# Kernel optimization log

Hardware: AMD Instinct MI355X
Metric: run time of the kernel (lower is better)

Reference implementation:

```python
import jax, jax.numpy as jnp
import numpy as np

H = 128          # hidden_size
GX = GY = 512    # grid_size
SW = 2           # spatial_width
NX = GX + 3 * SW # memory extent x (as in SpatialExternalMemory ctor)
NY = GY + 3 * SW
B = 512          # batch (num trajectories)
T = 64           # seq len (recurrent steps)


def setup_inputs() -> dict:
    key = jax.random.key(0)
    ks = jax.random.split(key, 9)
    stdv = 1.0 / np.sqrt(H)
    feat = jax.random.normal(ks[0], (B, T, 2), jnp.float32)
    # integer grid coords stored as floats in cols 2:4 (cast to long in forward)
    coords = jax.random.randint(ks[1], (B, T, 2), 0, GX).astype(jnp.float32)
    feature_tensor = jnp.concatenate([feat, coords], axis=-1)  # [B, T, 4]
    seq_lengths = jax.random.randint(ks[2], (B,), 1, T + 1)
    uni = lambda k, shp: jax.random.uniform(k, shp, jnp.float32, -stdv, stdv)
    return {
        "feature_tensor": feature_tensor,
        "W_ih": uni(ks[3], (4 * H, 2)),
        "b_ih": uni(ks[4], (4 * H,)),
        "W_hh": uni(ks[5], (4 * H, H)),
        "b_hh": uni(ks[6], (4 * H,)),
        "W_out": uni(ks[7], (H, 2 * H)),   # Attention.linear_out: [H, 2H]
        "b_out": uni(ks[8], (H,)),
        "seq_lengths": seq_lengths,
    }


def reference(feature_tensor, W_ih, b_ih, W_hh, b_hh, W_out, b_out, seq_lengths):
    step_idx = jnp.maximum(seq_lengths.astype(jnp.int32), 1) - 1  # [B]
    offsets = jnp.arange(-SW, SW + 1)                              # [K], K=2*SW+1
    K = 2 * SW + 1
    memory0 = jnp.zeros((NX, NY, H), jnp.float32)
    hidden0 = jnp.zeros((B, H), jnp.float32)
    last0 = jnp.zeros((B, H), jnp.float32)

    def step(carry, inp):
        hidden, memory, last = carry
        xt, t = inp                                 # xt: [B,4]
        feat = xt[:, :2]
        grid = xt[:, 2:4].astype(jnp.int32) + SW    # [B,2]
        gi = feat @ W_ih.T + b_ih                   # [B,4H]
        gh = hidden @ W_hh.T + b_hh                 # [B,4H]
        i_r, i_i, i_n, i_s = jnp.split(gi, 4, axis=1)
        h_r, h_i, h_n, h_s = jnp.split(gh, 4, axis=1)
        resetgate = jax.nn.sigmoid(i_r + h_r)
        updategate = jax.nn.sigmoid(i_i + h_i)
        spatialgate = jax.nn.sigmoid(i_s + h_s)
        newgate = jnp.tanh(i_n + resetgate * h_n)
        # --- find_nearby_grids: 5x5 neighborhood gather ---
        gx = jnp.clip(grid[:, 0], 0, NX - 1)
        gy = jnp.clip(grid[:, 1], 0, NY - 1)
        xi = jnp.clip(gx[:, None] + offsets[None, :], 0, NX - 1)   # [B,K]
        yi = jnp.clip(gy[:, None] + offsets[None, :], 0, NY - 1)   # [B,K]
        xg = jnp.broadcast_to(xi[:, :, None], (B, K, K)).reshape(B, K * K)
        yg = jnp.broadcast_to(yi[:, None, :], (B, K, K)).reshape(B, K * K)
        context = memory[xg, yg]                    # [B, K*K, H]
        # --- Attention(newgate.detach(), context) ---
        q = jax.lax.stop_gradient(newgate)
        scores = jnp.einsum('bh,bkh->bk', q, context)
        scores = jnp.where(scores == 0.0, -jnp.inf, scores)
        attn = jax.nn.softmax(scores, axis=1)
        attn = jnp.where(jnp.isnan(attn), 0.0, attn)
        mix = jnp.einsum('bk,bkh->bh', attn, context)
        atten_cs = jnp.tanh(jnp.concatenate([mix, q], axis=-1) @ W_out.T + b_out)
        curr = newgate + spatialgate * atten_cs
        out = curr + updategate * (hidden - curr)
        # --- in-cell memory write (detached, training-mode path) ---
        sd = jax.lax.stop_gradient(spatialgate)
        od = jax.lax.stop_gradient(out)
        upd = sd * memory[gx, gy] + (1.0 - sd) * od
        memory = memory.at[gx, gy].set(upd)
        last = jnp.where((step_idx == t)[:, None], out, last)
        return (out, memory, last), None

    xs = (jnp.swapaxes(feature_tensor, 0, 1), jnp.arange(T))
    (_, _, last), _ = jax.lax.scan(step, (hidden0, memory0, last0), xs)
    return last
```

## Files before the change

kernel.cpp:

```cpp
#include <hip/hip_runtime.h>
#include <hip/hip_fp16.h>
#include <math.h>

#define Hc   128
#define Bc   512
#define Tc   64
#define NXc  518
#define NCELL (518*518)
#define NEV  (Bc*Tc)
#define SWc  2


__global__ void k_build(const float* __restrict__ feat, int* __restrict__ head,
                        int* __restrict__ nxt, int* __restrict__ cellxy) {
    int gid = blockIdx.x * 256 + threadIdx.x;
    if (gid >= NEV) return;
    int b = gid >> 6, t = gid & 63;
    int base = (b * Tc + t) * 4;
    int gx = (int)feat[base + 2] + SWc;
    int gy = (int)feat[base + 3] + SWc;
    gx = min(max(gx, 0), NXc - 1);
    gy = min(max(gy, 0), NXc - 1);
    int cell = gx * NXc + gy;
    int e = t * Bc + b;
    cellxy[e] = (gx << 16) | gy;
    int old = atomicExch(&head[cell], e);
    nxt[e] = old;
}

__global__ void k_resolve(const int* __restrict__ head, const int* __restrict__ nxt,
                          const int* __restrict__ cellxy, int* __restrict__ dep) {
    int gid = blockIdx.x * 256 + threadIdx.x;
    if (gid >= NEV * 25) return;
    int r = gid / 25, k = gid - r * 25;
    int t = r & 63, b = r >> 6;
    int e0 = t * Bc + b;
    int xy = cellxy[e0];
    int gx = xy >> 16, gy = xy & 0xffff;
    int cx = gx + (k / 5) - SWc, cy = gy + (k % 5) - SWc;
    cx = min(max(cx, 0), NXc - 1);
    cy = min(max(cy, 0), NXc - 1);
    int cell = cx * NXc + cy;
    int best = -1;
    for (int e = head[cell]; e >= 0; e = nxt[e])
        if ((e >> 9) < t && e > best) best = e;
    dep[r * 25 + k] = best;
}


#define LOG2E 1.4426950408889634f
__device__ __forceinline__ float fexp(float x)  { return __builtin_amdgcn_exp2f(x * LOG2E); }
__device__ __forceinline__ float fsig(float x)  { return __builtin_amdgcn_rcpf(1.f + fexp(-x)); }
__device__ __forceinline__ float ftanh(float x) { return 1.f - 2.f * __builtin_amdgcn_rcpf(1.f + fexp(2.f * x)); }

__device__ __forceinline__ void barlds() {
    asm volatile("" ::: "memory");
    __builtin_amdgcn_s_waitcnt(0xC07F);
    __builtin_amdgcn_s_barrier();
    asm volatile("" ::: "memory");
}


constexpr int LDS_FLOATS = 16512 + 256 + 1024 + 256 + 256 + 256 + 64 + 2048 + 512 + 16 + 128 + 256 + 128;
constexpr int LDS_BYTES  = LDS_FLOATS * 4;

__global__ void
__attribute__((amdgpu_flat_work_group_size(1024, 1024)))
__attribute__((amdgpu_waves_per_eu(4, 4)))
step_main(const float* __restrict__ feat, const float* __restrict__ Wih,
          const float* __restrict__ bih,  const float* __restrict__ Whh,
          const float* __restrict__ bhh,  const float* __restrict__ Wout,
          const float* __restrict__ bout, const int*   __restrict__ seq,
          const int*   __restrict__ dep,  float* __restrict__ vbuf,
          unsigned*    __restrict__ flags, float* __restrict__ dout) {
    extern __shared__ float lds[];
    __half2* WoutH = (__half2*)lds;
    float* hid   = lds + 16512;
    float* g     = hid   + 256;
    float* gin   = g     + 1024;
    float* ctr   = gin   + 256;
    float* qvL   = ctr   + 256;
    float* scor  = qvL   + 256;
    float* pmix  = scor  + 64;
    float* catL  = pmix  + 2048;
    float* fxy   = catL  + 512;
    float* boutL = fxy   + 16;
    float* updL  = boutL + 128;
    int*   depv  = (int*)(updL + 256);

    const int tid  = threadIdx.x;
    const int blk  = blockIdx.x;
    const int lane = tid & 63;
    const int w    = tid >> 6;
    const int wj   = w >> 3;
    const int ww   = w & 7;

    const int o    = tid >> 1;
    const int half = tid & 1;
    float4 wr[16];
    {
        const float4* wp = (const float4*)(Whh + (size_t)o * Hc + half * 64);
        #pragma unroll
        for (int i = 0; i < 16; ++i) wr[i] = wp[i];
    }
    #pragma unroll
    for (int i = 0; i < 16; ++i)
        asm volatile("" : "+v"(wr[i].x), "+v"(wr[i].y), "+v"(wr[i].z), "+v"(wr[i].w));

    const float bihr = bih[o], bhhr = bhh[o];
    const float wih0 = Wih[o * 2 + 0], wih1 = Wih[o * 2 + 1];
    const int chunk = o >> 7;

    for (int i = tid; i < 128 * 128; i += 1024) {
        int r = i >> 7, c2 = i & 127;
        WoutH[r * 129 + c2] = __floats2half2_rn(Wout[r * 256 + 2 * c2],
                                                Wout[r * 256 + 2 * c2 + 1]);
    }
    if (tid < 128) boutL[tid] = bout[tid];
    if (tid < 256) hid[tid] = 0.f;
    if (tid < 8) { int j = tid >> 2, c = tid & 3;
                   fxy[tid] = feat[((size_t)(blk * 2 + j) * Tc + 0) * 4 + c]; }
    if (tid < 50) {
        int j = (tid >= 25), k = tid - j * 25;
        depv[tid] = dep[(((size_t)(blk * 2 + j)) * Tc + 0) * 25 + k];
    }
    const int s0 = max(seq[blk * 2 + 0], 1) - 1;
    const int s1 = max(seq[blk * 2 + 1], 1) - 1;
    __syncthreads();

    const float NEG_INF = -__builtin_inff();

    for (int t = 0; t < Tc; ++t) {
        const float* fx = fxy + (t & 1) * 8;
        int* depvCur = depv + (t & 1) * 64;
        int* depvNxt = depv + ((t + 1) & 1) * 64;

        if (t > 0 && (w == 0 || w == 2)) {
            int j = w >> 1;
            float2 u = *(const float2*)&updL[j * 128 + 2 * lane];
            unsigned long long raw; __builtin_memcpy(&raw, &u, 8);
            __hip_atomic_store((unsigned long long*)(vbuf +
                ((size_t)((t - 1) * Bc + blk * 2 + j)) * Hc + 2 * lane),
                raw, __ATOMIC_RELAXED, __HIP_MEMORY_SCOPE_AGENT);
        }
        const int mye = (lane < 25) ? depvCur[wj * 25 + lane] : -1;
        unsigned fpre = 1u;
        if (mye >= 0)
            fpre = __hip_atomic_load(&flags[mye], __ATOMIC_RELAXED,
                                     __HIP_MEMORY_SCOPE_AGENT);

        float acc0j, acc1j;
        {
            const float4* hp0 = (const float4*)(hid + half * 64);
            const float4* hp1 = (const float4*)(hid + 128 + half * 64);
            float a0 = 0.f, a1 = 0.f, a2 = 0.f, a3 = 0.f;
            float b0 = 0.f, b1 = 0.f, b2 = 0.f, b3 = 0.f;
            #pragma unroll
            for (int i = 0; i < 16; ++i) {
                float4 w4 = wr[i];
                float4 h0 = hp0[i], h1 = hp1[i];
                a0 = fmaf(w4.x, h0.x, a0); a1 = fmaf(w4.y, h0.y, a1);
                a2 = fmaf(w4.z, h0.z, a2); a3 = fmaf(w4.w, h0.w, a3);
                b0 = fmaf(w4.x, h1.x, b0); b1 = fmaf(w4.y, h1.y, b1);
                b2 = fmaf(w4.z, h1.z, b2); b3 = fmaf(w4.w, h1.w, b3);
            }
            acc0j = (a0 + a1) + (a2 + a3);
            acc1j = (b0 + b1) + (b2 + b3);
        }
        acc0j += __shfl_xor(acc0j, 1, 64);
        acc1j += __shfl_xor(acc1j, 1, 64);
        if (half == 0) {
            float gi0 = fmaf(wih0, fx[0], wih1 * fx[1]);
            float gi1 = fmaf(wih0, fx[4], wih1 * fx[5]);
            g[o]       = acc0j + bhhr + ((chunk == 2) ? 0.f : (gi0 + bihr));
            g[512 + o] = acc1j + bhhr + ((chunk == 2) ? 0.f : (gi1 + bihr));
            if (chunk == 2) { gin[o & 127] = gi0 + bihr; gin[128 + (o & 127)] = gi1 + bihr; }
        }
        if (tid >= 512 && tid < 562 && t + 1 < Tc) {
            int idx = tid - 512;
            int j = (idx >= 25), k = idx - j * 25;
            depvNxt[idx] = dep[(((size_t)(blk * 2 + j)) * Tc + (t + 1)) * 25 + k];
        }
        if (tid >= 960 && tid < 968 && t + 1 < Tc) {
            int idx = tid - 960, j = idx >> 2, c = idx & 3;
            fxy[((t + 1) & 1) * 8 + idx] =
                feat[((size_t)(blk * 2 + j) * Tc + (t + 1)) * 4 + c];
        }
        if (t > 0 && (w == 0 || w == 2)) {
            asm volatile("s_waitcnt vmcnt(0)" ::: "memory");
            if (lane == 0)
                __hip_atomic_store(&flags[(t - 1) * Bc + blk * 2 + (w >> 1)], 1u,
                                   __ATOMIC_RELAXED, __HIP_MEMORY_SCOPE_AGENT);
        }
        {
            bool pend = (mye >= 0) && (fpre == 0u);
            while (__any(pend)) {
                if (pend && __hip_atomic_load(&flags[mye], __ATOMIC_RELAXED,
                                              __HIP_MEMORY_SCOPE_AGENT) != 0u)
                    pend = false;
                if (__any(pend)) __builtin_amdgcn_s_sleep(1);
            }
        }
        asm volatile("" ::: "memory");
        float2 valk[4];
        int    evk[4];
        #pragma unroll
        for (int kk = 0; kk < 4; ++kk) {
            int k = ww + 8 * kk;
            evk[kk] = (k < 25) ? depvCur[wj * 25 + k] : -1;
            valk[kk] = make_float2(0.f, 0.f);
            if (evk[kk] >= 0)
                valk[kk] = *(const float2*)(vbuf + (size_t)evk[kk] * Hc + 2 * lane);
        }
        barlds();

        float q0, q1;
        {
            float2 gr2 = *(const float2*)&g[wj * 512 + 2 * lane];
            float2 gn2 = *(const float2*)&g[wj * 512 + 256 + 2 * lane];
            float2 gi2 = *(const float2*)&gin[wj * 128 + 2 * lane];
            q0 = ftanh(gi2.x + fsig(gr2.x) * gn2.x);
            q1 = ftanh(gi2.y + fsig(gr2.y) * gn2.y);
        }
        if (ww == 0) *(float2*)&qvL[wj * 128 + 2 * lane] = make_float2(q0, q1);
        if (ww == 4)
            *(float2*)&ctr[wj * 128 + 2 * lane] =
                (evk[1] >= 0) ? valk[1] : make_float2(0.f, 0.f);
        #pragma unroll
        for (int kk = 0; kk < 4; ++kk) {
            int k = ww + 8 * kk;
            if (k < 25) {
                float sc;
                if (evk[kk] >= 0) {
                    float d = fmaf(valk[kk].x, q0, valk[kk].y * q1);
                    #pragma unroll
                    for (int m = 1; m < 64; m <<= 1) d += __shfl_xor(d, m, 64);
                    sc = (d == 0.f) ? NEG_INF : d;
                } else sc = NEG_INF;
                if (lane == 0) scor[wj * 32 + k] = sc;
            }
        }
        barlds();

        {
            int k2 = lane & 31;
            float v = (k2 < 25) ? scor[wj * 32 + k2] : NEG_INF;
            float m = v;
            #pragma unroll
            for (int mm = 1; mm < 32; mm <<= 1) m = fmaxf(m, __shfl_xor(m, mm, 64));
            float a = 0.f;
            if (m != NEG_INF) {
                float p = (v == NEG_INF) ? 0.f : fexp(v - m);
                float s = p;
                #pragma unroll
                for (int mm = 1; mm < 32; mm <<= 1) s += __shfl_xor(s, mm, 64);
                a = p / s;
            }
            float pm0 = 0.f, pm1 = 0.f;
            #pragma unroll
            for (int kk = 0; kk < 4; ++kk) {
                int k = ww + 8 * kk;
                if (k < 25 && evk[kk] >= 0) {
                    float ak = __shfl(a, k, 64);
                    pm0 = fmaf(ak, valk[kk].x, pm0);
                    pm1 = fmaf(ak, valk[kk].y, pm1);
                }
            }
            *(float2*)&pmix[(wj * 8 + ww) * 128 + 2 * lane] = make_float2(pm0, pm1);
        }
        barlds();

        if (tid < 256) {
            int j = tid >> 7, h = tid & 127;
            float mix = 0.f;
            #pragma unroll
            for (int p = 0; p < 8; ++p) mix += pmix[(j * 8 + p) * 128 + h];
            catL[j * 256 + h] = mix;
            catL[j * 256 + 128 + h] = qvL[j * 128 + h];
        }
        barlds();

        {
            int oo = tid & 127, rep = tid >> 7;
            const __half2* wrow = WoutH + oo * 129 + rep * 16;
            const float4* c04 = (const float4*)(catL + rep * 32);
            const float4* c14 = (const float4*)(catL + 256 + rep * 32);
            float acc0 = 0.f, acc1 = 0.f;
            #pragma unroll
            for (int i = 0; i < 8; ++i) {
                __half2 wa = wrow[2 * i], wb = wrow[2 * i + 1];
                float wx = __low2float(wa), wy = __high2float(wa);
                float wz = __low2float(wb), wwv = __high2float(wb);
                float4 c0 = c04[i], c1 = c14[i];
                acc0 = fmaf(wx, c0.x, fmaf(wy, c0.y, fmaf(wz, c0.z, fmaf(wwv, c0.w, acc0))));
                acc1 = fmaf(wx, c1.x, fmaf(wy, c1.y, fmaf(wz, c1.z, fmaf(wwv, c1.w, acc1))));
            }
            pmix[rep * 128 + oo]       = acc0;
            pmix[(8 + rep) * 128 + oo] = acc1;
        }
        barlds();

        if (tid < 256) {
            int j = tid >> 7, h = tid & 127;
            float tot = boutL[h];
            #pragma unroll
            for (int p = 0; p < 8; ++p) tot += pmix[(j * 8 + p) * 128 + h];
            float at = ftanh(tot);
            float gr = g[j * 512 + h],       gu = g[j * 512 + 128 + h];
            float gn = g[j * 512 + 256 + h], gs = g[j * 512 + 384 + h];
            float rr = fsig(gr), uu = fsig(gu), ss = fsig(gs);
            float nn = ftanh(gin[j * 128 + h] + rr * gn);
            float hv = hid[j * 128 + h];
            float curr = fmaf(ss, at, nn);
            float outv = curr + uu * (hv - curr);
            hid[j * 128 + h] = outv;
            if (t < Tc - 1)
                updL[tid] = fmaf(ss, ctr[j * 128 + h], (1.f - ss) * outv);
            int sj = (j == 0) ? s0 : s1;
            if (sj == t) dout[(size_t)(blk * 2 + j) * Hc + h] = outv;
        }
        barlds();
    }
}


extern "C" void kernel_launch(void* const* d_in, const int* in_sizes, int n_in,
                              void* d_out, int out_size, void* d_ws, size_t ws_size,
                              hipStream_t stream) {
    const float* feat = (const float*)d_in[0];
    const float* Wih  = (const float*)d_in[1];
    const float* bih  = (const float*)d_in[2];
    const float* Whh  = (const float*)d_in[3];
    const float* bhh  = (const float*)d_in[4];
    const float* Wout = (const float*)d_in[5];
    const float* bout = (const float*)d_in[6];
    const int*   seq  = (const int*)d_in[7];

    char* ws = (char*)d_ws;
    size_t off = 0;
    auto carve = [&](size_t bytes) { char* p = ws + off; off += (bytes + 511) & ~(size_t)511; return p; };
    float*    vbuf   = (float*)   carve((size_t)NEV * Hc * 4);
    int*      head   = (int*)     carve((size_t)NCELL * 4);
    int*      nxt    = (int*)     carve((size_t)NEV * 4);
    int*      cellxy = (int*)     carve((size_t)NEV * 4);
    int*      dep    = (int*)     carve((size_t)NEV * 25 * 4);
    unsigned* flags  = (unsigned*)carve((size_t)NEV * 4);

    hipMemsetAsync(head, 0xFF, (size_t)NCELL * 4, stream);
    hipMemsetAsync(flags, 0, (size_t)NEV * 4, stream);

    k_build<<<(NEV + 255) / 256, 256, 0, stream>>>(feat, head, nxt, cellxy);
    k_resolve<<<(NEV * 25 + 255) / 256, 256, 0, stream>>>(head, nxt, cellxy, dep);

    hipFuncSetAttribute((const void*)step_main,
                        hipFuncAttributeMaxDynamicSharedMemorySize, LDS_BYTES);
    step_main<<<256, 1024, LDS_BYTES, stream>>>(feat, Wih, bih, Whh, bhh, Wout, bout,
                                                seq, dep, vbuf, flags, (float*)d_out);
}
```

Measured before the change: 515.7 us.

## Use DPP/swizzle wave reductions and 4-lane split for recurrent matvec

Replaces the shuffle-based wave reductions in the attention score, softmax max and sum with DPP row ops plus ds_swizzle, and uses readlane instead of a shuffle to broadcast attention weights. The W_hh matvec is reorganised so each group of four lanes holds two weight rows with interleaved column slices, which cuts the cross-lane reduction to two DPP adds. This aims to lower latency in the serial per-step critical path, at the cost of trickier DPP control codes and a changed LDS access pattern for the hidden vector reads.

Result: faster. 459.1 us (-11.0%).

```diff
diff --git a/kernel.cpp b/kernel.cpp
--- a/kernel.cpp
+++ b/kernel.cpp
@@ -52,6 +52,27 @@
 __device__ __forceinline__ float fexp(float x)  { return __builtin_amdgcn_exp2f(x * LOG2E); }
 __device__ __forceinline__ float fsig(float x)  { return __builtin_amdgcn_rcpf(1.f + fexp(-x)); }
 __device__ __forceinline__ float ftanh(float x) { return 1.f - 2.f * __builtin_amdgcn_rcpf(1.f + fexp(2.f * x)); }
+
+template <int CTRL>
+__device__ __forceinline__ float dppadd(float x) {
+    int t = __builtin_amdgcn_update_dpp(0, __float_as_int(x), CTRL, 0xF, 0xF, true);
+    return x + __int_as_float(t);
+}
+template <int CTRL>
+__device__ __forceinline__ float dppmax(float x) {
+    int t = __builtin_amdgcn_update_dpp(0, __float_as_int(x), CTRL, 0xF, 0xF, true);
+    return fmaxf(x, __int_as_float(t));
+}
+__device__ __forceinline__ float swz16(float x) {
+    return __int_as_float(__builtin_amdgcn_ds_swizzle(__float_as_int(x), 0x401F));
+}
+__device__ __forceinline__ float redsum64(float d) {
+    d = dppadd<0xB1>(d); d = dppadd<0x4E>(d);
+    d = dppadd<0x141>(d); d = dppadd<0x140>(d);
+    d += swz16(d);
+    d += __shfl_xor(d, 32, 64);
+    return d;
+}
 
 __device__ __forceinline__ void barlds() {
     asm volatile("" ::: "memory");
@@ -95,21 +116,26 @@
     const int wj   = w >> 3;
     const int ww   = w & 7;
 
-    const int o    = tid >> 1;
-    const int half = tid & 1;
-    float4 wr[16];
+    const int rp = tid >> 2;
+    const int q  = tid & 3;
+    const int r0 = 2 * rp, r1 = 2 * rp + 1;
+    float4 wr0[8], wr1[8];
     {
-        const float4* wp = (const float4*)(Whh + (size_t)o * Hc + half * 64);
+        const float4* w0 = (const float4*)(Whh + (size_t)r0 * Hc);
+        const float4* w1 = (const float4*)(Whh + (size_t)r1 * Hc);
         #pragma unroll
-        for (int i = 0; i < 16; ++i) wr[i] = wp[i];
+        for (int i = 0; i < 8; ++i) { wr0[i] = w0[q + 4 * i]; wr1[i] = w1[q + 4 * i]; }
     }
     #pragma unroll
-    for (int i = 0; i < 16; ++i)
-        asm volatile("" : "+v"(wr[i].x), "+v"(wr[i].y), "+v"(wr[i].z), "+v"(wr[i].w));
-
-    const float bihr = bih[o], bhhr = bhh[o];
-    const float wih0 = Wih[o * 2 + 0], wih1 = Wih[o * 2 + 1];
-    const int chunk = o >> 7;
+    for (int i = 0; i < 8; ++i) {
+        asm volatile("" : "+v"(wr0[i].x), "+v"(wr0[i].y), "+v"(wr0[i].z), "+v"(wr0[i].w));
+        asm volatile("" : "+v"(wr1[i].x), "+v"(wr1[i].y), "+v"(wr1[i].z), "+v"(wr1[i].w));
+    }
+    const int jw = q & 1;
+    const int rw = r0 + (q >> 1);
+    const float bihr = bih[rw], bhhr = bhh[rw];
+    const float wihA = Wih[rw * 2 + 0], wihB = Wih[rw * 2 + 1];
+    const int chunk = rw >> 7;
 
     for (int i = tid; i < 128 * 128; i += 1024) {
         int r = i >> 7, c2 = i & 127;
@@ -149,32 +175,29 @@
             fpre = __hip_atomic_load(&flags[mye], __ATOMIC_RELAXED,
                                      __HIP_MEMORY_SCOPE_AGENT);
 
-        float acc0j, acc1j;
-        {
-            const float4* hp0 = (const float4*)(hid + half * 64);
-            const float4* hp1 = (const float4*)(hid + 128 + half * 64);
-            float a0 = 0.f, a1 = 0.f, a2 = 0.f, a3 = 0.f;
-            float b0 = 0.f, b1 = 0.f, b2 = 0.f, b3 = 0.f;
-            #pragma unroll
-            for (int i = 0; i < 16; ++i) {
-                float4 w4 = wr[i];
-                float4 h0 = hp0[i], h1 = hp1[i];
-                a0 = fmaf(w4.x, h0.x, a0); a1 = fmaf(w4.y, h0.y, a1);
-                a2 = fmaf(w4.z, h0.z, a2); a3 = fmaf(w4.w, h0.w, a3);
-                b0 = fmaf(w4.x, h1.x, b0); b1 = fmaf(w4.y, h1.y, b1);
-                b2 = fmaf(w4.z, h1.z, b2); b3 = fmaf(w4.w, h1.w, b3);
-            }
-            acc0j = (a0 + a1) + (a2 + a3);
-            acc1j = (b0 + b1) + (b2 + b3);
-        }
-        acc0j += __shfl_xor(acc0j, 1, 64);
-        acc1j += __shfl_xor(acc1j, 1, 64);
-        if (half == 0) {
-            float gi0 = fmaf(wih0, fx[0], wih1 * fx[1]);
-            float gi1 = fmaf(wih0, fx[4], wih1 * fx[5]);
-            g[o]       = acc0j + bhhr + ((chunk == 2) ? 0.f : (gi0 + bihr));
-            g[512 + o] = acc1j + bhhr + ((chunk == 2) ? 0.f : (gi1 + bihr));
-            if (chunk == 2) { gin[o & 127] = gi0 + bihr; gin[128 + (o & 127)] = gi1 + bihr; }
+        float a00 = 0.f, a01 = 0.f, a10 = 0.f, a11 = 0.f;
+        {
+            const float4* h0 = (const float4*)hid;
+            const float4* h1 = (const float4*)(hid + 128);
+            #pragma unroll
+            for (int i = 0; i < 8; ++i) {
+                float4 hv0 = h0[q + 4 * i], hv1 = h1[q + 4 * i];
+                float4 w0 = wr0[i], w1 = wr1[i];
+                a00 = fmaf(w0.x, hv0.x, fmaf(w0.y, hv0.y, fmaf(w0.z, hv0.z, fmaf(w0.w, hv0.w, a00))));
+                a01 = fmaf(w1.x, hv0.x, fmaf(w1.y, hv0.y, fmaf(w1.z, hv0.z, fmaf(w1.w, hv0.w, a01))));
+                a10 = fmaf(w0.x, hv1.x, fmaf(w0.y, hv1.y, fmaf(w0.z, hv1.z, fmaf(w0.w, hv1.w, a10))));
+                a11 = fmaf(w1.x, hv1.x, fmaf(w1.y, hv1.y, fmaf(w1.z, hv1.z, fmaf(w1.w, hv1.w, a11))));
+            }
+        }
+        a00 = dppadd<0x4E>(dppadd<0xB1>(a00));
+        a01 = dppadd<0x4E>(dppadd<0xB1>(a01));
+        a10 = dppadd<0x4E>(dppadd<0xB1>(a10));
+        a11 = dppadd<0x4E>(dppadd<0xB1>(a11));
+        {
+            float mine = (q & 1) ? ((q >> 1) ? a11 : a10) : ((q >> 1) ? a01 : a00);
+            float gi  = fmaf(wihA, fx[jw * 4 + 0], wihB * fx[jw * 4 + 1]);
+            g[jw * 512 + rw] = mine + bhhr + ((chunk == 2) ? 0.f : (gi + bihr));
+            if (chunk == 2) gin[jw * 128 + (rw & 127)] = gi + bihr;
         }
         if (tid >= 512 && tid < 562 && t + 1 < Tc) {
             int idx = tid - 512;
@@ -233,8 +256,7 @@
                 float sc;
                 if (evk[kk] >= 0) {
                     float d = fmaf(valk[kk].x, q0, valk[kk].y * q1);
-                    #pragma unroll
-                    for (int m = 1; m < 64; m <<= 1) d += __shfl_xor(d, m, 64);
+                    d = redsum64(d);
                     sc = (d == 0.f) ? NEG_INF : d;
                 } else sc = NEG_INF;
                 if (lane == 0) scor[wj * 32 + k] = sc;
@@ -246,14 +268,16 @@
             int k2 = lane & 31;
             float v = (k2 < 25) ? scor[wj * 32 + k2] : NEG_INF;
             float m = v;
-            #pragma unroll
-            for (int mm = 1; mm < 32; mm <<= 1) m = fmaxf(m, __shfl_xor(m, mm, 64));
+            m = dppmax<0xB1>(m); m = dppmax<0x4E>(m);
+            m = dppmax<0x141>(m); m = dppmax<0x140>(m);
+            m = fmaxf(m, swz16(m));
             float a = 0.f;
             if (m != NEG_INF) {
                 float p = (v == NEG_INF) ? 0.f : fexp(v - m);
                 float s = p;
-                #pragma unroll
-                for (int mm = 1; mm < 32; mm <<= 1) s += __shfl_xor(s, mm, 64);
+                s = dppadd<0xB1>(s); s = dppadd<0x4E>(s);
+                s = dppadd<0x141>(s); s = dppadd<0x140>(s);
+                s += swz16(s);
                 a = p / s;
             }
             float pm0 = 0.f, pm1 = 0.f;
@@ -261,7 +285,8 @@
             for (int kk = 0; kk < 4; ++kk) {
                 int k = ww + 8 * kk;
                 if (k < 25 && evk[kk] >= 0) {
-                    float ak = __shfl(a, k, 64);
+                    float ak = __int_as_float(
+                        __builtin_amdgcn_readlane(__float_as_int(a), k));
                     pm0 = fmaf(ak, valk[kk].x, pm0);
                     pm1 = fmaf(ak, valk[kk].y, pm1);
                 }
```
